# Optimization experiments

Measured on AMD Instinct MI355X. Metric: run time of the kernel, lower is better.

Reference implementation:

```python
import jax, jax.numpy as jnp
import numpy as np

N, E, H, NH, HD = 16384, 131072, 128, 8, 16
CUTOFF = 5.0
PATCH = H // 2  # 64, aggregation_custom effective patch dim


def setup_inputs() -> dict:
    key = jax.random.key(0)
    ks = jax.random.split(key, 24)
    w = lambda k, s: (jax.random.normal(k, s, dtype=jnp.float32) * 0.05)
    d = jax.random.normal(ks[5], (E, 3), dtype=jnp.float32)
    d = d / (jnp.linalg.norm(d, axis=-1, keepdims=True) + 1e-8)  # unit directions
    return {
        "x": jax.random.normal(ks[0], (N, H), dtype=jnp.float32),
        "vec": jax.random.normal(ks[1], (N, 3, H), dtype=jnp.float32),
        "edge_index": jax.random.randint(ks[2], (2, E), 0, N),
        "r_ij": jax.random.uniform(ks[3], (E,), dtype=jnp.float32) * CUTOFF,
        "f_ij": jax.random.normal(ks[4], (E, H), dtype=jnp.float32),
        "d_ij": d,
        "ln_g": jnp.ones((H,), jnp.float32), "ln_b": jnp.zeros((H,), jnp.float32),
        "Wq": w(ks[6], (H, H)), "bq": jnp.zeros((H,), jnp.float32),
        "Wk": w(ks[7], (H, H)), "bk": jnp.zeros((H,), jnp.float32),
        "Wv": w(ks[8], (H, H)), "bv": jnp.zeros((H,), jnp.float32),
        "Wdk": w(ks[9], (H, H)), "bdk": jnp.zeros((H,), jnp.float32),
        "Wdv": w(ks[10], (H, H)), "bdv": jnp.zeros((H,), jnp.float32),
        "Wvec": w(ks[11], (3 * H, H)),
        "Ws": w(ks[12], (2 * H, H)), "bs": jnp.zeros((2 * H,), jnp.float32),
        "Wo": w(ks[13], (3 * H, H)), "bo": jnp.zeros((3 * H,), jnp.float32),
        "Wf": w(ks[14], (H, H)), "bf": jnp.zeros((H,), jnp.float32),
        "Wwsrc": w(ks[15], (H, H)), "Wwtrg": w(ks[16], (H, H)),
        "Wagg": w(ks[17], (H, PATCH)),  # fc_all: Linear(64 -> 128, no bias)
        "agg_param": jnp.full((1,), 1e-5, dtype=jnp.float32),
    }


def _cutoff(r):
    return 0.5 * (jnp.cos(jnp.pi * r / CUTOFF) + 1.0) * (r < CUTOFF).astype(r.dtype)


def _vector_rejection(v, d):
    # v: [E,3,H], d: [E,3]
    proj = (v * d[:, :, None]).sum(axis=1, keepdims=True)  # [E,1,H]
    return v - proj * d[:, :, None]


def reference(x, vec, edge_index, r_ij, f_ij, d_ij, ln_g, ln_b,
              Wq, bq, Wk, bk, Wv, bv, Wdk, bdk, Wdv, bdv, Wvec,
              Ws, bs, Wo, bo, Wf, bf, Wwsrc, Wwtrg, Wagg, agg_param):
    silu = jax.nn.silu
    n = x.shape[0]
    # LayerNorm on x; VecLayerNorm with norm_type='none', trainable=False is identity
    mu = x.mean(-1, keepdims=True)
    var = ((x - mu) ** 2).mean(-1, keepdims=True)
    xn = (x - mu) / jnp.sqrt(var + 1e-5) * ln_g + ln_b

    q = (xn @ Wq.T + bq).reshape(n, NH, HD)
    k = (xn @ Wk.T + bk).reshape(n, NH, HD)
    v = (xn @ Wv.T + bv).reshape(n, NH, HD)
    dk = silu(f_ij @ Wdk.T + bdk).reshape(-1, NH, HD)
    dv = silu(f_ij @ Wdv.T + bdv).reshape(-1, NH, HD)

    vec1, vec2, vec3 = jnp.split(jnp.einsum('nch,oh->nco', vec, Wvec), 3, axis=-1)
    vec_dot = (vec1 * vec2).sum(axis=1)  # [N,H]

    src, dst = edge_index[0], edge_index[1]  # j, i
    # --- message ---
    attn = (q[dst] * k[src] * dk).sum(-1)                      # [E,NH]
    attn = silu(attn) * _cutoff(r_ij)[:, None]
    vmsg = (v[src] * dv * attn[:, :, None]).reshape(-1, H)     # [E,H]
    s1, s2 = jnp.split(silu(vmsg @ Ws.T + bs), 2, axis=1)
    vec_msg = vec[src] * s1[:, None, :] + s2[:, None, :] * d_ij[:, :, None]  # [E,3,H]

    # --- aggregation_custom on scalar messages ---
    e = vmsg.reshape(-1, 2, PATCH)                 # [E,2,64]
    ex = jnp.clip(jnp.einsum('epd,od->epo', e, Wagg), 0.0, 1.0)  # [E,2,128]
    gated = jnp.concatenate([(e * ex[:, :, :PATCH]).sum(1),
                             (e * ex[:, :, PATCH:]).sum(1)], axis=-1)  # [E,128]
    x_orig = jax.ops.segment_sum(vmsg, dst, num_segments=n)
    x_gate = jax.ops.segment_sum(gated, dst, num_segments=n)
    x_agg = jnp.abs(agg_param) * x_gate + x_orig
    vec_agg = jax.ops.segment_sum(vec_msg.reshape(-1, 3 * H), dst, num_segments=n).reshape(n, 3, H)

    # --- update ---
    o1, o2, o3 = jnp.split(x_agg @ Wo.T + bo, 3, axis=1)
    dx = vec_dot * o2 + o3
    dvec = vec3 * o1[:, None, :] + vec_agg

    # --- edge_update ---
    w1 = _vector_rejection(jnp.einsum('ech,oh->eco', vec[dst], Wwtrg), d_ij)
    w2 = _vector_rejection(jnp.einsum('ech,oh->eco', vec[src], Wwsrc), -d_ij)
    w_dot = (w1 * w2).sum(axis=1)  # [E,H]
    df_ij = silu(f_ij @ Wf.T + bf) * w_dot
    return dx, dvec, df_ij
```

## Files before the change

### kernel.cpp

```cpp
#include <hip/hip_runtime.h>

#define NN 16384
#define NE 131072
#define HH 128

typedef unsigned short u16;
typedef unsigned int u32;
typedef __attribute__((ext_vector_type(8))) short short8;
typedef __attribute__((ext_vector_type(4))) float f32x4;
typedef __attribute__((ext_vector_type(2))) float f32x2;
typedef __attribute__((ext_vector_type(2))) u32 u32x2;

__device__ __forceinline__ float b2f(u16 u){ u32 i=((u32)u)<<16; float f; __builtin_memcpy(&f,&i,4); return f; }
__device__ __forceinline__ u16 f2b(float f){ u32 i; __builtin_memcpy(&i,&f,4); u32 r=(i+0x7fffu+((i>>16)&1u))>>16; return (u16)r; }
__device__ __forceinline__ float blo(u32 v){ return b2f((u16)(v&0xffffu)); }
__device__ __forceinline__ float bhi(u32 v){ return b2f((u16)(v>>16)); }
__device__ __forceinline__ u32 pk(float a, float b){ return (u32)f2b(a) | ((u32)f2b(b)<<16); }
__device__ __forceinline__ float siluf(float x){ return x/(1.f+__expf(-x)); }

#define PBASE 58720256u
enum : unsigned {
  O_Wq=PBASE+0, O_Wk=PBASE+16384, O_Wv=PBASE+32768, O_Wdk=PBASE+49152,
  O_Wdv=PBASE+65536, O_Wf=PBASE+81920, O_Wwsrc=PBASE+98304, O_Wwtrg=PBASE+114688,
  O_Wvec=PBASE+131072, O_Ws=PBASE+180224, O_Wo=PBASE+212992, O_Wagg=PBASE+262144,
  O_bq=PBASE+270336, O_bk=PBASE+270464, O_bv=PBASE+270592, O_bdk=PBASE+270720,
  O_bdv=PBASE+270848, O_bs=PBASE+270976, O_bo=PBASE+271232, O_bf=PBASE+271616,
  O_lng=PBASE+271744, O_lnb=PBASE+271872, O_agg=PBASE+272000
};
#define CNT_OFF 117985280u
#define CUR_OFF 118050816u
#define SE_OFF  118116352u

struct Seg { const float* s; u32 off; u32 n; };
struct Pack { Seg d[25]; int cnt; };

__global__ __launch_bounds__(256) void k_cvt(Pack p, u16* __restrict__ base){
  int tid = blockIdx.x*blockDim.x + threadIdx.x;
  int stride = gridDim.x*blockDim.x;
  for (int s=0; s<p.cnt; ++s){
    const float* src = p.d[s].s;
    u16* dst = base + p.d[s].off;
    int n = (int)p.d[s].n, n4 = n>>2;
    const f32x4* s4 = (const f32x4*)src;
    for (int i=tid; i<n4; i+=stride){
      f32x4 v = s4[i];
      u32x2 o; o[0] = pk(v[0], v[1]); o[1] = pk(v[2], v[3]);
      *(u32x2*)(dst + 4*(size_t)i) = o;
    }
    for (int i = n4*4 + tid; i < n; i += stride) dst[i] = f2b(src[i]);
  }
}

__global__ __launch_bounds__(256) void k_hist(const int* __restrict__ ei, int* __restrict__ cnt){
  int e = blockIdx.x*256 + threadIdx.x;
  atomicAdd(&cnt[ei[NE + e]], 1);
}
__global__ __launch_bounds__(1024) void k_scan(const int* __restrict__ cnt, int* __restrict__ cur){
  __shared__ int part[1024];
  int t = threadIdx.x;
  int base = t*16;
  int local[16]; int s = 0;
#pragma unroll
  for (int k=0;k<16;++k){ local[k] = cnt[base+k]; s += local[k]; }
  part[t] = s;
  __syncthreads();
  for (int d=1; d<1024; d<<=1){
    int v = (t>=d) ? part[t-d] : 0;
    __syncthreads();
    part[t] += v;
    __syncthreads();
  }
  int run = (t>0) ? part[t-1] : 0;
#pragma unroll
  for (int k=0;k<16;++k){ cur[base+k] = run; run += local[k]; }
}
__global__ __launch_bounds__(256) void k_place(const int* __restrict__ ei, int* __restrict__ cur,
                                               int* __restrict__ se){
  int e = blockIdx.x*256 + threadIdx.x;
  int p = atomicAdd(&cur[ei[NE + e]], 1);
  se[p] = e;
}

template<int NK>
__device__ __forceinline__ f32x4 mm16(const u16* A, int lda, const u16* W, int ldw, f32x4 acc){
  int lane = threadIdx.x & 63;
  const u16* pa = A + (lane & 15)*lda + ((lane>>4)<<3);
  const u16* pw = W + (lane & 15)*ldw + ((lane>>4)<<3);
#pragma unroll
  for (int kc = 0; kc < NK; ++kc){
    short8 a = *(const short8*)(pa + kc*32);
    short8 b = *(const short8*)(pw + kc*32);
    acc = __builtin_amdgcn_mfma_f32_16x16x32_bf16(a, b, acc, 0, 0, 0);
  }
  return acc;
}

__global__ __launch_bounds__(256) void k_ln(const float* __restrict__ x, const u16* __restrict__ pb,
                                            u16* __restrict__ xn){
  int wid = threadIdx.x>>6, lane = threadIdx.x & 63;
  int n = blockIdx.x*4 + wid;
  f32x2 v = *(const f32x2*)(x + (size_t)n*HH + 2*lane);
  float a0 = v[0], a1 = v[1];
  float s = a0 + a1;
#pragma unroll
  for (int m=32; m; m>>=1) s += __shfl_xor(s, m);
  float mu = s*(1.f/128.f);
  float d0 = a0-mu, d1 = a1-mu;
  float vs = d0*d0 + d1*d1;
#pragma unroll
  for (int m=32; m; m>>=1) vs += __shfl_xor(vs, m);
  float rs = rsqrtf(vs*(1.f/128.f) + 1e-5f);
  u32 gg = *(const u32*)(pb + O_lng + 2*lane);
  u32 bb = *(const u32*)(pb + O_lnb + 2*lane);
  *(u32*)(xn + (size_t)n*HH + 2*lane) = pk(d0*rs*blo(gg)+blo(bb), d1*rs*bhi(gg)+bhi(bb));
}

__global__ __launch_bounds__(256) void k_gemm_qkv(const u16* __restrict__ xn,
    const u16* __restrict__ pb, u16* __restrict__ qkv){
  int wid = threadIdx.x>>6, lane = threadIdx.x & 63;
  int ct = blockIdx.y*4 + wid;
  int r0 = blockIdx.x*16;
  unsigned wo, bo_;
  if (ct < 8)      { wo = O_Wq; bo_ = O_bq; }
  else if (ct <16) { wo = O_Wk; bo_ = O_bk; }
  else             { wo = O_Wv; bo_ = O_bv; }
  int c0 = (ct & 7)*16;
  f32x4 acc = {0,0,0,0};
  acc = mm16<4>(xn + (size_t)r0*HH, HH, pb + wo + c0*HH, HH, acc);
  int col = ct*16 + (lane & 15);
  float bb = b2f(pb[bo_ + c0 + (lane&15)]);
#pragma unroll
  for (int j=0;j<4;++j){
    int r = r0 + ((lane>>4)<<2) + j;
    qkv[(size_t)r*384 + col] = f2b(acc[j] + bb);
  }
}

__global__ __launch_bounds__(256) void k_gemm_vec(const float* __restrict__ vecf,
    const u16* __restrict__ pb,
    u16* __restrict__ v12, u16* __restrict__ vec3, u16* __restrict__ Y){
  __shared__ u16 At[16*128];
  int tid = threadIdx.x, wid = tid>>6, lane = tid & 63;
  int r0 = blockIdx.x*16;
  {
    const float* src = vecf + (size_t)r0*HH;
    for (int i = tid*4; i < 2048; i += 1024){
      f32x4 v = *(const f32x4*)(src + i);
      u32x2 o; o[0] = pk(v[0], v[1]); o[1] = pk(v[2], v[3]);
      *(u32x2*)(At + i) = o;
    }
  }
  __syncthreads();
  for (int ct = wid; ct < 40; ct += 4){
    unsigned wo; int wc0;
    if (ct < 24)      { wo = O_Wvec;  wc0 = ct*16; }
    else if (ct < 32) { wo = O_Wwsrc; wc0 = (ct-24)*16; }
    else              { wo = O_Wwtrg; wc0 = (ct-32)*16; }
    f32x4 acc = {0,0,0,0};
    acc = mm16<4>(At, HH, pb + wo + wc0*HH, HH, acc);
    u16* dst; int ldc, dc0;
    if (ct < 16)      { dst = v12;  ldc = 256; dc0 = ct*16; }
    else if (ct < 24) { dst = vec3; ldc = 128; dc0 = (ct-16)*16; }
    else if (ct < 32) { dst = Y;    ldc = 256; dc0 = (ct-24)*16; }
    else              { dst = Y;    ldc = 256; dc0 = (ct-32)*16 + 128; }
    int col = dc0 + (lane & 15);
#pragma unroll
    for (int j=0;j<4;++j){
      int r = r0 + ((lane>>4)<<2) + j;
      dst[(size_t)r*ldc + col] = f2b(acc[j]);
    }
  }
}

__global__ __launch_bounds__(256) void k_edge(const float* __restrict__ f_ij,
    const u16* __restrict__ pb,
    const u16* __restrict__ qkv, const u16* __restrict__ Y,
    const int* __restrict__ ei, const int* __restrict__ se,
    const float* __restrict__ r_ij, const float* __restrict__ d_ij,
    const float* __restrict__ vecf, const float* __restrict__ aggf,
    float* __restrict__ df, float* __restrict__ xacc, float* __restrict__ vacc){
  __shared__ u16 fs[64*128];
  __shared__ u16 g2s[64*256];
  int tid = threadIdx.x, wid = tid>>6, lane = tid & 63;
  int t0 = blockIdx.x*64;
  int ereg=0, dreg=0, sreg=0;
  if (lane < 16){
    ereg = se[t0 + wid*16 + lane];
    dreg = ei[NE + ereg];
    sreg = ei[ereg];
  }
#pragma unroll
  for (int pass=0; pass<8; ++pass){
    int idx = pass*256 + lane*4;
    int rloc = idx >> 7, col = idx & 127;
    int er = __shfl(ereg, rloc);
    f32x4 v = *(const f32x4*)(f_ij + (size_t)er*HH + col);
    u32x2 o; o[0]=pk(v[0],v[1]); o[1]=pk(v[2],v[3]);
    *(u32x2*)(fs + (wid*16 + rloc)*HH + col) = o;
  }
  {
    const u16* pa = fs + (size_t)(wid*16 + (lane&15))*HH + ((lane>>4)<<3);
    short8 a0 = *(const short8*)(pa);
    short8 a1 = *(const short8*)(pa + 32);
    short8 a2 = *(const short8*)(pa + 64);
    short8 a3 = *(const short8*)(pa + 96);
    for (int ct=0; ct<16; ++ct){
      unsigned wo  = (ct<8) ? O_Wdk : O_Wdv;
      unsigned bo_ = (ct<8) ? O_bdk : O_bdv;
      int c0 = (ct&7)*16;
      const u16* pw = pb + wo + (size_t)(c0 + (lane&15))*HH + ((lane>>4)<<3);
      f32x4 acc = {0,0,0,0};
      acc = __builtin_amdgcn_mfma_f32_16x16x32_bf16(a0, *(const short8*)(pw),      acc, 0,0,0);
      acc = __builtin_amdgcn_mfma_f32_16x16x32_bf16(a1, *(const short8*)(pw + 32), acc, 0,0,0);
      acc = __builtin_amdgcn_mfma_f32_16x16x32_bf16(a2, *(const short8*)(pw + 64), acc, 0,0,0);
      acc = __builtin_amdgcn_mfma_f32_16x16x32_bf16(a3, *(const short8*)(pw + 96), acc, 0,0,0);
      float bb = b2f(pb[bo_ + c0 + (lane&15)]);
#pragma unroll
      for (int j=0;j<4;++j){
        int r = wid*16 + ((lane>>4)<<2) + j;
        g2s[r*256 + ct*16 + (lane&15)] = f2b(siluf(acc[j] + bb));
      }
    }
    f32x4 ffa[8];
#pragma unroll
    for (int cf=0; cf<8; ++cf){
      const u16* pw = pb + O_Wf + (size_t)(cf*16 + (lane&15))*HH + ((lane>>4)<<3);
      f32x4 acc = {0,0,0,0};
      acc = __builtin_amdgcn_mfma_f32_16x16x32_bf16(a0, *(const short8*)(pw),      acc, 0,0,0);
      acc = __builtin_amdgcn_mfma_f32_16x16x32_bf16(a1, *(const short8*)(pw + 32), acc, 0,0,0);
      acc = __builtin_amdgcn_mfma_f32_16x16x32_bf16(a2, *(const short8*)(pw + 64), acc, 0,0,0);
      acc = __builtin_amdgcn_mfma_f32_16x16x32_bf16(a3, *(const short8*)(pw + 96), acc, 0,0,0);
      ffa[cf] = acc;
    }
#pragma unroll
    for (int cf=0; cf<8; ++cf){
      float bb = b2f(pb[O_bf + cf*16 + (lane&15)]);
#pragma unroll
      for (int j=0;j<4;++j){
        int r = wid*16 + ((lane>>4)<<2) + j;
        fs[r*HH + cf*16 + (lane&15)] = f2b(siluf(ffa[cf][j] + bb));
      }
    }
  }
  int h0 = 2*lane;
  {
    int pdst = -1; u32 qq=0, ya0=0, ya1=0, ya2=0;
    for (int i=0;i<16;++i){
      int el = wid*16 + i;
      int e   = __shfl(ereg, i);
      int dst = __shfl(dreg, i);
      int src = __shfl(sreg, i);
      if (dst != pdst){
        qq  = *(const u32*)(qkv + (size_t)dst*384 + h0);
        ya0 = *(const u32*)(Y + ((size_t)dst*3+0)*256 + 128 + h0);
        ya1 = *(const u32*)(Y + ((size_t)dst*3+1)*256 + 128 + h0);
        ya2 = *(const u32*)(Y + ((size_t)dst*3+2)*256 + 128 + h0);
        pdst = dst;
      }
      u32 kk = *(const u32*)(qkv + (size_t)src*384 + 128 + h0);
      u32 vv = *(const u32*)(qkv + (size_t)src*384 + 256 + h0);
      u32 dk = *(const u32*)(g2s + el*256 + h0);
      u32 dv = *(const u32*)(g2s + el*256 + 128 + h0);
      u32 ff = *(const u32*)(fs  + el*HH + h0);
      float p = blo(qq)*blo(kk)*blo(dk) + bhi(qq)*bhi(kk)*bhi(dk);
      p += __shfl_xor(p,1); p += __shfl_xor(p,2); p += __shfl_xor(p,4);
      float r = r_ij[e];
      float cut = 0.5f*(__cosf(0.6283185307f*r)+1.f) * (r < 5.f ? 1.f : 0.f);
      float attn = siluf(p)*cut;
      float m0 = blo(vv)*blo(dv)*attn, m1 = bhi(vv)*bhi(dv)*attn;
      float ab0=0,ab1=0, ad0=0,ad1=0, bd0=0,bd1=0, ss=0;
      u32 ya[3] = {ya0, ya1, ya2};
#pragma unroll
      for (int c=0;c<3;++c){
        u32 bv2 = *(const u32*)(Y + ((size_t)src*3+c)*256 + h0);
        float dc = d_ij[(size_t)e*3+c];
        ab0 += blo(ya[c])*blo(bv2); ab1 += bhi(ya[c])*bhi(bv2);
        ad0 += blo(ya[c])*dc;       ad1 += bhi(ya[c])*dc;
        bd0 += blo(bv2)*dc;         bd1 += bhi(bv2)*dc;
        ss  += dc*dc;
      }
      float t = 2.f - ss;
      f32x2 dfo; dfo[0] = blo(ff)*(ab0 - ad0*bd0*t); dfo[1] = bhi(ff)*(ab1 - ad1*bd1*t);
      *(f32x2*)(df + (size_t)e*HH + h0) = dfo;
      *(u32*)(fs + el*HH + h0) = pk(m0, m1);
    }
  }
  float absA = fabsf(aggf[0]);
#pragma unroll
  for (int rr=0; rr<2; ++rr){
    int rt = wid*2 + rr;
    int el2 = wid*16 + 8*rr + ((lane&15)>>1);
    const u16* pa2 = fs + (size_t)el2*HH + ((lane&15)&1)*64 + ((lane>>4)<<3);
    short8 b0 = *(const short8*)(pa2);
    short8 b1 = *(const short8*)(pa2 + 32);
    for (int ct=0; ct<8; ++ct){
      const u16* pw = pb + O_Wagg + (size_t)(ct*16 + (lane&15))*64 + ((lane>>4)<<3);
      f32x4 acc = {0,0,0,0};
      acc = __builtin_amdgcn_mfma_f32_16x16x32_bf16(b0, *(const short8*)(pw),      acc, 0,0,0);
      acc = __builtin_amdgcn_mfma_f32_16x16x32_bf16(b1, *(const short8*)(pw + 32), acc, 0,0,0);
#pragma unroll
      for (int j=0;j<4;++j){
        int r = rt*16 + ((lane>>4)<<2) + j;
        g2s[r*128 + ct*16 + (lane&15)] = f2b(fminf(fmaxf(acc[j],0.f),1.f));
      }
    }
  }
  {
    int rdst = -1; float xc0=0.f, xc1=0.f;
    for (int i=0;i<16;++i){
      int el = wid*16 + i;
      int dst = __shfl(dreg, i);
      if (dst != rdst){
        if (rdst >= 0){
          atomicAdd(&xacc[(size_t)rdst*HH + h0],     xc0);
          atomicAdd(&xacc[(size_t)rdst*HH + h0 + 1], xc1);
        }
        rdst = dst; xc0 = xc1 = 0.f;
      }
      u32 mm = *(const u32*)(fs + el*HH + h0);
      u32 ml = *(const u32*)(fs + el*HH + (h0 & 63));
      u32 mh = *(const u32*)(fs + el*HH + 64 + (h0 & 63));
      u32 ex0 = *(const u32*)(g2s + (2*el)*128 + h0);
      u32 ex1 = *(const u32*)(g2s + (2*el+1)*128 + h0);
      xc0 += blo(mm) + absA*(blo(ml)*blo(ex0) + blo(mh)*blo(ex1));
      xc1 += bhi(mm) + absA*(bhi(ml)*bhi(ex0) + bhi(mh)*bhi(ex1));
    }
    if (rdst >= 0){
      atomicAdd(&xacc[(size_t)rdst*HH + h0],     xc0);
      atomicAdd(&xacc[(size_t)rdst*HH + h0 + 1], xc1);
    }
  }
  {
    const u16* ps = fs + (size_t)(wid*16 + (lane&15))*HH + ((lane>>4)<<3);
    short8 sa0 = *(const short8*)(ps);
    short8 sa1 = *(const short8*)(ps + 32);
    short8 sa2 = *(const short8*)(ps + 64);
    short8 sa3 = *(const short8*)(ps + 96);
    for (int ct=0; ct<16; ++ct){
      const u16* pw = pb + O_Ws + (size_t)(ct*16 + (lane&15))*HH + ((lane>>4)<<3);
      f32x4 acc = {0,0,0,0};
      acc = __builtin_amdgcn_mfma_f32_16x16x32_bf16(sa0, *(const short8*)(pw),      acc, 0,0,0);
      acc = __builtin_amdgcn_mfma_f32_16x16x32_bf16(sa1, *(const short8*)(pw + 32), acc, 0,0,0);
      acc = __builtin_amdgcn_mfma_f32_16x16x32_bf16(sa2, *(const short8*)(pw + 64), acc, 0,0,0);
      acc = __builtin_amdgcn_mfma_f32_16x16x32_bf16(sa3, *(const short8*)(pw + 96), acc, 0,0,0);
      float bb = b2f(pb[O_bs + ct*16 + (lane&15)]);
#pragma unroll
      for (int j=0;j<4;++j){
        int r = wid*16 + ((lane>>4)<<2) + j;
        g2s[r*256 + ct*16 + (lane&15)] = f2b(siluf(acc[j] + bb));
      }
    }
  }
  {
    int rdst = -1;
    float vc00=0.f,vc01=0.f, vc10=0.f,vc11=0.f, vc20=0.f,vc21=0.f;
    for (int i=0;i<16;++i){
      int el = wid*16 + i;
      int e   = __shfl(ereg, i);
      int dst = __shfl(dreg, i);
      int src = __shfl(sreg, i);
      if (dst != rdst){
        if (rdst >= 0){
          atomicAdd(&vacc[((size_t)rdst*3+0)*HH + h0],     vc00);
          atomicAdd(&vacc[((size_t)rdst*3+0)*HH + h0 + 1], vc01);
          atomicAdd(&vacc[((size_t)rdst*3+1)*HH + h0],     vc10);
          atomicAdd(&vacc[((size_t)rdst*3+1)*HH + h0 + 1], vc11);
          atomicAdd(&vacc[((size_t)rdst*3+2)*HH + h0],     vc20);
          atomicAdd(&vacc[((size_t)rdst*3+2)*HH + h0 + 1], vc21);
        }
        rdst = dst;
        vc00=vc01=vc10=vc11=vc20=vc21=0.f;
      }
      u32 s1 = *(const u32*)(g2s + el*256 + h0);
      u32 s2 = *(const u32*)(g2s + el*256 + 128 + h0);
      f32x2 vv0 = *(const f32x2*)(vecf + ((size_t)src*3+0)*HH + h0);
      f32x2 vv1 = *(const f32x2*)(vecf + ((size_t)src*3+1)*HH + h0);
      f32x2 vv2 = *(const f32x2*)(vecf + ((size_t)src*3+2)*HH + h0);
      float dc0 = d_ij[(size_t)e*3+0], dc1 = d_ij[(size_t)e*3+1], dc2 = d_ij[(size_t)e*3+2];
      vc00 += vv0[0]*blo(s1) + blo(s2)*dc0;  vc01 += vv0[1]*bhi(s1) + bhi(s2)*dc0;
      vc10 += vv1[0]*blo(s1) + blo(s2)*dc1;  vc11 += vv1[1]*bhi(s1) + bhi(s2)*dc1;
      vc20 += vv2[0]*blo(s1) + blo(s2)*dc2;  vc21 += vv2[1]*bhi(s1) + bhi(s2)*dc2;
    }
    if (rdst >= 0){
      atomicAdd(&vacc[((size_t)rdst*3+0)*HH + h0],     vc00);
      atomicAdd(&vacc[((size_t)rdst*3+0)*HH + h0 + 1], vc01);
      atomicAdd(&vacc[((size_t)rdst*3+1)*HH + h0],     vc10);
      atomicAdd(&vacc[((size_t)rdst*3+1)*HH + h0 + 1], vc11);
      atomicAdd(&vacc[((size_t)rdst*3+2)*HH + h0],     vc20);
      atomicAdd(&vacc[((size_t)rdst*3+2)*HH + h0 + 1], vc21);
    }
  }
}

__global__ __launch_bounds__(256) void k_update(const float* __restrict__ xacc,
    const u16* __restrict__ pb, const u16* __restrict__ v12, const u16* __restrict__ vec3,
    const float* __restrict__ vacc,
    float* __restrict__ dx, float* __restrict__ dvec){
  int wid = threadIdx.x>>6, lane = threadIdx.x & 63;
  int ct = blockIdx.y*4 + wid;
  int r0 = blockIdx.x*16;
  int c0 = ct*16;
  f32x4 a1 = {0,0,0,0}, a2 = {0,0,0,0}, a3 = {0,0,0,0};
  const float* pa = xacc + (size_t)(r0 + (lane&15))*HH + ((lane>>4)<<3);
#pragma unroll
  for (int kc=0; kc<4; ++kc){
    f32x4 f0 = *(const f32x4*)(pa + kc*32);
    f32x4 f1 = *(const f32x4*)(pa + kc*32 + 4);
    short8 av;
    av[0]=(short)f2b(f0[0]); av[1]=(short)f2b(f0[1]); av[2]=(short)f2b(f0[2]); av[3]=(short)f2b(f0[3]);
    av[4]=(short)f2b(f1[0]); av[5]=(short)f2b(f1[1]); av[6]=(short)f2b(f1[2]); av[7]=(short)f2b(f1[3]);
    const u16* pw = pb + O_Wo + (size_t)(c0 + (lane&15))*HH + ((lane>>4)<<3) + kc*32;
    short8 b1 = *(const short8*)(pw);
    short8 b2 = *(const short8*)(pw + 128*HH);
    short8 b3 = *(const short8*)(pw + 256*HH);
    a1 = __builtin_amdgcn_mfma_f32_16x16x32_bf16(av, b1, a1, 0,0,0);
    a2 = __builtin_amdgcn_mfma_f32_16x16x32_bf16(av, b2, a2, 0,0,0);
    a3 = __builtin_amdgcn_mfma_f32_16x16x32_bf16(av, b3, a3, 0,0,0);
  }
  int h = c0 + (lane & 15);
  float bo1 = b2f(pb[O_bo + h]), bo2 = b2f(pb[O_bo + 128 + h]), bo3 = b2f(pb[O_bo + 256 + h]);
#pragma unroll
  for (int j=0;j<4;++j){
    int r = r0 + ((lane>>4)<<2) + j;
    float o1 = a1[j]+bo1, o2 = a2[j]+bo2, o3 = a3[j]+bo3;
    float vdot = 0.f;
#pragma unroll
    for (int c=0;c<3;++c){
      const u16* row = v12 + ((size_t)r*3 + c)*256;
      vdot += b2f(row[h]) * b2f(row[128 + h]);
    }
    dx[(size_t)r*HH + h] = vdot*o2 + o3;
#pragma unroll
    for (int c=0;c<3;++c){
      size_t idx = ((size_t)r*3+c)*HH + h;
      dvec[idx] = b2f(vec3[idx])*o1 + vacc[idx];
    }
  }
}

extern "C" void kernel_launch(void* const* d_in, const int* in_sizes, int n_in,
                              void* d_out, int out_size, void* d_ws, size_t ws_size,
                              hipStream_t stream){
  (void)in_sizes; (void)n_in; (void)out_size; (void)ws_size;
  const float* x     = (const float*)d_in[0];
  const float* vecf  = (const float*)d_in[1];
  const int*   ei    = (const int*)d_in[2];
  const float* r_ij  = (const float*)d_in[3];
  const float* f_ij  = (const float*)d_in[4];
  const float* d_ij  = (const float*)d_in[5];
  const float* aggf  = (const float*)d_in[28];

  char* ws = (char*)d_ws;
  u16*   wsu   = (u16*)d_ws;
  float* xacc  = (float*)(ws + 0);
  float* vacc  = (float*)(ws + 8388608);
  u16*   Ybuf  = (u16*)(ws + 33554432);
  u16*   xn    = (u16*)(ws + 58720256);
  u16*   vec3  = (u16*)(ws + 67108864);
  u16*   qkv   = (u16*)(ws + 79691776);
  u16*   v12   = (u16*)(ws + 92274688);
  int*   cnt   = (int*)(ws + CNT_OFF);
  int*   cur   = (int*)(ws + CUR_OFF);
  int*   se    = (int*)(ws + SE_OFF);

  float* out  = (float*)d_out;
  float* dx   = out;
  float* dvec = out + (size_t)NN*128;
  float* df   = out + (size_t)NN*512;

  Pack p; int c = 0;
  auto add = [&](int idx, unsigned off, unsigned n){ p.d[c].s=(const float*)d_in[idx]; p.d[c].off=off; p.d[c].n=n; ++c; };
  add(8,  O_Wq,   16384); add(10, O_Wk,   16384); add(12, O_Wv,   16384);
  add(14, O_Wdk,  16384); add(16, O_Wdv,  16384); add(23, O_Wf,   16384);
  add(25, O_Wwsrc,16384); add(26, O_Wwtrg,16384);
  add(18, O_Wvec, 49152); add(19, O_Ws,   32768); add(21, O_Wo,   49152);
  add(27, O_Wagg,  8192);
  add(9,  O_bq, 128); add(11, O_bk, 128); add(13, O_bv, 128); add(15, O_bdk, 128);
  add(17, O_bdv, 128); add(20, O_bs, 256); add(22, O_bo, 384); add(24, O_bf, 128);
  add(6,  O_lng, 128); add(7,  O_lnb, 128); add(28, O_agg, 1);
  p.cnt = c;

  hipMemsetAsync(ws, 0, 33554432, stream);
  hipMemsetAsync(ws + CNT_OFF, 0, 65536, stream);
  k_hist<<<dim3(NE/256), 256, 0, stream>>>(ei, cnt);
  k_scan<<<dim3(1), 1024, 0, stream>>>(cnt, cur);
  k_place<<<dim3(NE/256), 256, 0, stream>>>(ei, cur, se);
  k_cvt<<<dim3(128), 256, 0, stream>>>(p, wsu);
  k_ln<<<dim3(NN/4), 256, 0, stream>>>(x, wsu, xn);
  k_gemm_qkv<<<dim3(NN/16, 6), 256, 0, stream>>>(xn, wsu, qkv);
  k_gemm_vec<<<dim3(3*NN/16), 256, 0, stream>>>(vecf, wsu, v12, vec3, Ybuf);
  k_edge<<<dim3(NE/64), 256, 0, stream>>>(f_ij, wsu, qkv, Ybuf, ei, se, r_ij, d_ij,
                                          vecf, aggf, df, xacc, vacc);
  k_update<<<dim3(NN/16, 2), 256, 0, stream>>>(xacc, wsu, v12, vec3, vacc, dx, dvec);
}
```

Baseline: 428.6 us.

## Swizzle LDS tiles and software-prefetch per-edge gathers in edge kernel

Applies an XOR swizzle to the byte addresses of the shared-memory tiles fs and g2s so that the MFMA fragment reads and the strided stores spread across LDS banks. It also prefetches the next edge's source-node gathers (k, v, Y, vec) and its r_ij and d_ij values one iteration ahead in the two per-edge loops, hiding global load latency. The prefetch adds register pressure, which could lower occupancy, and the swizzle adds a little address arithmetic.

```diff
diff --git a/kernel.cpp b/kernel.cpp
--- a/kernel.cpp
+++ b/kernel.cpp
@@ -17,6 +17,9 @@
 __device__ __forceinline__ float bhi(u32 v){ return b2f((u16)(v>>16)); }
 __device__ __forceinline__ u32 pk(float a, float b){ return (u32)f2b(a) | ((u32)f2b(b)<<16); }
 __device__ __forceinline__ float siluf(float x){ return x/(1.f+__expf(-x)); }
+
+#define SW8(b) ((b) ^ ((((b)>>8)&7)<<4))
+#define SW9(b) ((b) ^ ((((b)>>9)&7)<<4))
 
 #define PBASE 58720256u
 enum : unsigned {
@@ -181,6 +184,8 @@
     float* __restrict__ df, float* __restrict__ xacc, float* __restrict__ vacc){
   __shared__ u16 fs[64*128];
   __shared__ u16 g2s[64*256];
+  char* fsb  = (char*)fs;
+  char* g2b  = (char*)g2s;
   int tid = threadIdx.x, wid = tid>>6, lane = tid & 63;
   int t0 = blockIdx.x*64;
   int ereg=0, dreg=0, sreg=0;
@@ -196,14 +201,16 @@
     int er = __shfl(ereg, rloc);
     f32x4 v = *(const f32x4*)(f_ij + (size_t)er*HH + col);
     u32x2 o; o[0]=pk(v[0],v[1]); o[1]=pk(v[2],v[3]);
-    *(u32x2*)(fs + (wid*16 + rloc)*HH + col) = o;
+    int b = (wid*16 + rloc)*256 + col*2;
+    *(u32x2*)(fsb + SW8(b)) = o;
   }
   {
-    const u16* pa = fs + (size_t)(wid*16 + (lane&15))*HH + ((lane>>4)<<3);
-    short8 a0 = *(const short8*)(pa);
-    short8 a1 = *(const short8*)(pa + 32);
-    short8 a2 = *(const short8*)(pa + 64);
-    short8 a3 = *(const short8*)(pa + 96);
+    int arow = wid*16 + (lane&15);
+    int ab = arow*256 + ((lane>>4)<<4);
+    short8 a0 = *(const short8*)(fsb + SW8(ab));
+    short8 a1 = *(const short8*)(fsb + SW8(ab + 64));
+    short8 a2 = *(const short8*)(fsb + SW8(ab + 128));
+    short8 a3 = *(const short8*)(fsb + SW8(ab + 192));
     for (int ct=0; ct<16; ++ct){
       unsigned wo  = (ct<8) ? O_Wdk : O_Wdv;
       unsigned bo_ = (ct<8) ? O_bdk : O_bdv;
@@ -218,7 +225,8 @@
 #pragma unroll
       for (int j=0;j<4;++j){
         int r = wid*16 + ((lane>>4)<<2) + j;
-        g2s[r*256 + ct*16 + (lane&15)] = f2b(siluf(acc[j] + bb));
+        int b = r*512 + (ct*16 + (lane&15))*2;
+        *(u16*)(g2b + SW9(b)) = f2b(siluf(acc[j] + bb));
       }
     }
     f32x4 ffa[8];
@@ -238,18 +246,43 @@
 #pragma unroll
       for (int j=0;j<4;++j){
         int r = wid*16 + ((lane>>4)<<2) + j;
-        fs[r*HH + cf*16 + (lane&15)] = f2b(siluf(ffa[cf][j] + bb));
+        int b = r*256 + (cf*16 + (lane&15))*2;
+        *(u16*)(fsb + SW8(b)) = f2b(siluf(ffa[cf][j] + bb));
       }
     }
   }
   int h0 = 2*lane;
   {
     int pdst = -1; u32 qq=0, ya0=0, ya1=0, ya2=0;
+    int e_c = __shfl(ereg, 0), src_c = __shfl(sreg, 0);
+    u32 kk_c  = *(const u32*)(qkv + (size_t)src_c*384 + 128 + h0);
+    u32 vv_c  = *(const u32*)(qkv + (size_t)src_c*384 + 256 + h0);
+    u32 yb0_c = *(const u32*)(Y + ((size_t)src_c*3+0)*256 + h0);
+    u32 yb1_c = *(const u32*)(Y + ((size_t)src_c*3+1)*256 + h0);
+    u32 yb2_c = *(const u32*)(Y + ((size_t)src_c*3+2)*256 + h0);
+    float r_c   = r_ij[e_c];
+    float dc0_c = d_ij[(size_t)e_c*3+0];
+    float dc1_c = d_ij[(size_t)e_c*3+1];
+    float dc2_c = d_ij[(size_t)e_c*3+2];
     for (int i=0;i<16;++i){
+      int e = e_c;
+      u32 kk=kk_c, vv=vv_c, yb0=yb0_c, yb1=yb1_c, yb2=yb2_c;
+      float r=r_c, dc0=dc0_c, dc1=dc1_c, dc2=dc2_c;
+      if (i<15){
+        int e_n = __shfl(ereg, i+1), src_n = __shfl(sreg, i+1);
+        kk_c  = *(const u32*)(qkv + (size_t)src_n*384 + 128 + h0);
+        vv_c  = *(const u32*)(qkv + (size_t)src_n*384 + 256 + h0);
+        yb0_c = *(const u32*)(Y + ((size_t)src_n*3+0)*256 + h0);
+        yb1_c = *(const u32*)(Y + ((size_t)src_n*3+1)*256 + h0);
+        yb2_c = *(const u32*)(Y + ((size_t)src_n*3+2)*256 + h0);
+        r_c   = r_ij[e_n];
+        dc0_c = d_ij[(size_t)e_n*3+0];
+        dc1_c = d_ij[(size_t)e_n*3+1];
+        dc2_c = d_ij[(size_t)e_n*3+2];
+        e_c = e_n;
+      }
       int el = wid*16 + i;
-      int e   = __shfl(ereg, i);
       int dst = __shfl(dreg, i);
-      int src = __shfl(sreg, i);
       if (dst != pdst){
         qq  = *(const u32*)(qkv + (size_t)dst*384 + h0);
         ya0 = *(const u32*)(Y + ((size_t)dst*3+0)*256 + 128 + h0);
@@ -257,32 +290,33 @@
         ya2 = *(const u32*)(Y + ((size_t)dst*3+2)*256 + 128 + h0);
         pdst = dst;
       }
-      u32 kk = *(const u32*)(qkv + (size_t)src*384 + 128 + h0);
-      u32 vv = *(const u32*)(qkv + (size_t)src*384 + 256 + h0);
-      u32 dk = *(const u32*)(g2s + el*256 + h0);
-      u32 dv = *(const u32*)(g2s + el*256 + 128 + h0);
-      u32 ff = *(const u32*)(fs  + el*HH + h0);
+      int bdk = el*512 + h0*2;
+      u32 dk = *(const u32*)(g2b + SW9(bdk));
+      u32 dv = *(const u32*)(g2b + SW9(bdk + 256));
+      int bff = el*256 + h0*2;
+      u32 ff = *(const u32*)(fsb + SW8(bff));
       float p = blo(qq)*blo(kk)*blo(dk) + bhi(qq)*bhi(kk)*bhi(dk);
       p += __shfl_xor(p,1); p += __shfl_xor(p,2); p += __shfl_xor(p,4);
-      float r = r_ij[e];
       float cut = 0.5f*(__cosf(0.6283185307f*r)+1.f) * (r < 5.f ? 1.f : 0.f);
       float attn = siluf(p)*cut;
       float m0 = blo(vv)*blo(dv)*attn, m1 = bhi(vv)*bhi(dv)*attn;
-      float ab0=0,ab1=0, ad0=0,ad1=0, bd0=0,bd1=0, ss=0;
-      u32 ya[3] = {ya0, ya1, ya2};
-#pragma unroll
-      for (int c=0;c<3;++c){
-        u32 bv2 = *(const u32*)(Y + ((size_t)src*3+c)*256 + h0);
-        float dc = d_ij[(size_t)e*3+c];
-        ab0 += blo(ya[c])*blo(bv2); ab1 += bhi(ya[c])*bhi(bv2);
-        ad0 += blo(ya[c])*dc;       ad1 += bhi(ya[c])*dc;
-        bd0 += blo(bv2)*dc;         bd1 += bhi(bv2)*dc;
-        ss  += dc*dc;
-      }
+      float ab0,ab1, ad0,ad1, bd0,bd1, ss;
+      ab0 = blo(ya0)*blo(yb0); ab1 = bhi(ya0)*bhi(yb0);
+      ad0 = blo(ya0)*dc0;      ad1 = bhi(ya0)*dc0;
+      bd0 = blo(yb0)*dc0;      bd1 = bhi(yb0)*dc0;
+      ss  = dc0*dc0;
+      ab0 += blo(ya1)*blo(yb1); ab1 += bhi(ya1)*bhi(yb1);
+      ad0 += blo(ya1)*dc1;      ad1 += bhi(ya1)*dc1;
+      bd0 += blo(yb1)*dc1;      bd1 += bhi(yb1)*dc1;
+      ss  += dc1*dc1;
+      ab0 += blo(ya2)*blo(yb2); ab1 += bhi(ya2)*bhi(yb2);
+      ad0 += blo(ya2)*dc2;      ad1 += bhi(ya2)*dc2;
+      bd0 += blo(yb2)*dc2;      bd1 += bhi(yb2)*dc2;
+      ss  += dc2*dc2;
       float t = 2.f - ss;
       f32x2 dfo; dfo[0] = blo(ff)*(ab0 - ad0*bd0*t); dfo[1] = bhi(ff)*(ab1 - ad1*bd1*t);
       *(f32x2*)(df + (size_t)e*HH + h0) = dfo;
-      *(u32*)(fs + el*HH + h0) = pk(m0, m1);
+      *(u32*)(fsb + SW8(bff)) = pk(m0, m1);
     }
   }
   float absA = fabsf(aggf[0]);
@@ -290,9 +324,9 @@
   for (int rr=0; rr<2; ++rr){
     int rt = wid*2 + rr;
     int el2 = wid*16 + 8*rr + ((lane&15)>>1);
-    const u16* pa2 = fs + (size_t)el2*HH + ((lane&15)&1)*64 + ((lane>>4)<<3);
-    short8 b0 = *(const short8*)(pa2);
-    short8 b1 = *(const short8*)(pa2 + 32);
+    int pb2 = el2*256 + ((lane&15)&1)*128 + ((lane>>4)<<4);
+    short8 b0 = *(const short8*)(fsb + SW8(pb2));
+    short8 b1 = *(const short8*)(fsb + SW8(pb2 + 64));
     for (int ct=0; ct<8; ++ct){
       const u16* pw = pb + O_Wagg + (size_t)(ct*16 + (lane&15))*64 + ((lane>>4)<<3);
       f32x4 acc = {0,0,0,0};
@@ -301,7 +335,8 @@
 #pragma unroll
       for (int j=0;j<4;++j){
         int r = rt*16 + ((lane>>4)<<2) + j;
-        g2s[r*128 + ct*16 + (lane&15)] = f2b(fminf(fmaxf(acc[j],0.f),1.f));
+        int b = r*256 + (ct*16 + (lane&15))*2;
+        *(u16*)(g2b + SW8(b)) = f2b(fminf(fmaxf(acc[j],0.f),1.f));
       }
     }
   }
@@ -317,11 +352,12 @@
         }
         rdst = dst; xc0 = xc1 = 0.f;
       }
-      u32 mm = *(const u32*)(fs + el*HH + h0);
-      u32 ml = *(const u32*)(fs + el*HH + (h0 & 63));
-      u32 mh = *(const u32*)(fs + el*HH + 64 + (h0 & 63));
-      u32 ex0 = *(const u32*)(g2s + (2*el)*128 + h0);
-      u32 ex1 = *(const u32*)(g2s + (2*el+1)*128 + h0);
+      int bm = el*256;
+      u32 mm = *(const u32*)(fsb + SW8(bm + h0*2));
+      u32 ml = *(const u32*)(fsb + SW8(bm + (h0&63)*2));
+      u32 mh = *(const u32*)(fsb + SW8(bm + 128 + (h0&63)*2));
+      u32 ex0 = *(const u32*)(g2b + SW8((2*el)*256 + h0*2));
+      u32 ex1 = *(const u32*)(g2b + SW8((2*el+1)*256 + h0*2));
       xc0 += blo(mm) + absA*(blo(ml)*blo(ex0) + blo(mh)*blo(ex1));
       xc1 += bhi(mm) + absA*(bhi(ml)*bhi(ex0) + bhi(mh)*bhi(ex1));
     }
@@ -331,11 +367,12 @@
     }
   }
   {
-    const u16* ps = fs + (size_t)(wid*16 + (lane&15))*HH + ((lane>>4)<<3);
-    short8 sa0 = *(const short8*)(ps);
-    short8 sa1 = *(const short8*)(ps + 32);
-    short8 sa2 = *(const short8*)(ps + 64);
-    short8 sa3 = *(const short8*)(ps + 96);
+    int arow = wid*16 + (lane&15);
+    int ab = arow*256 + ((lane>>4)<<4);
+    short8 sa0 = *(const short8*)(fsb + SW8(ab));
+    short8 sa1 = *(const short8*)(fsb + SW8(ab + 64));
+    short8 sa2 = *(const short8*)(fsb + SW8(ab + 128));
+    short8 sa3 = *(const short8*)(fsb + SW8(ab + 192));
     for (int ct=0; ct<16; ++ct){
       const u16* pw = pb + O_Ws + (size_t)(ct*16 + (lane&15))*HH + ((lane>>4)<<3);
       f32x4 acc = {0,0,0,0};
@@ -347,18 +384,35 @@
 #pragma unroll
       for (int j=0;j<4;++j){
         int r = wid*16 + ((lane>>4)<<2) + j;
-        g2s[r*256 + ct*16 + (lane&15)] = f2b(siluf(acc[j] + bb));
+        int b = r*512 + (ct*16 + (lane&15))*2;
+        *(u16*)(g2b + SW9(b)) = f2b(siluf(acc[j] + bb));
       }
     }
   }
   {
     int rdst = -1;
     float vc00=0.f,vc01=0.f, vc10=0.f,vc11=0.f, vc20=0.f,vc21=0.f;
+    int e_c = __shfl(ereg, 0), src_c = __shfl(sreg, 0);
+    f32x2 v0_c = *(const f32x2*)(vecf + ((size_t)src_c*3+0)*HH + h0);
+    f32x2 v1_c = *(const f32x2*)(vecf + ((size_t)src_c*3+1)*HH + h0);
+    f32x2 v2_c = *(const f32x2*)(vecf + ((size_t)src_c*3+2)*HH + h0);
+    float dc0_c = d_ij[(size_t)e_c*3+0];
+    float dc1_c = d_ij[(size_t)e_c*3+1];
+    float dc2_c = d_ij[(size_t)e_c*3+2];
     for (int i=0;i<16;++i){
+      f32x2 vv0=v0_c, vv1=v1_c, vv2=v2_c;
+      float dc0=dc0_c, dc1=dc1_c, dc2=dc2_c;
+      if (i<15){
+        int e_n = __shfl(ereg, i+1), src_n = __shfl(sreg, i+1);
+        v0_c = *(const f32x2*)(vecf + ((size_t)src_n*3+0)*HH + h0);
+        v1_c = *(const f32x2*)(vecf + ((size_t)src_n*3+1)*HH + h0);
+        v2_c = *(const f32x2*)(vecf + ((size_t)src_n*3+2)*HH + h0);
+        dc0_c = d_ij[(size_t)e_n*3+0];
+        dc1_c = d_ij[(size_t)e_n*3+1];
+        dc2_c = d_ij[(size_t)e_n*3+2];
+      }
       int el = wid*16 + i;
-      int e   = __shfl(ereg, i);
       int dst = __shfl(dreg, i);
-      int src = __shfl(sreg, i);
       if (dst != rdst){
         if (rdst >= 0){
           atomicAdd(&vacc[((size_t)rdst*3+0)*HH + h0],     vc00);
@@ -371,12 +425,9 @@
         rdst = dst;
         vc00=vc01=vc10=vc11=vc20=vc21=0.f;
       }
-      u32 s1 = *(const u32*)(g2s + el*256 + h0);
-      u32 s2 = *(const u32*)(g2s + el*256 + 128 + h0);
-      f32x2 vv0 = *(const f32x2*)(vecf + ((size_t)src*3+0)*HH + h0);
-      f32x2 vv1 = *(const f32x2*)(vecf + ((size_t)src*3+1)*HH + h0);
-      f32x2 vv2 = *(const f32x2*)(vecf + ((size_t)src*3+2)*HH + h0);
-      float dc0 = d_ij[(size_t)e*3+0], dc1 = d_ij[(size_t)e*3+1], dc2 = d_ij[(size_t)e*3+2];
+      int bs1 = el*512 + h0*2;
+      u32 s1 = *(const u32*)(g2b + SW9(bs1));
+      u32 s2 = *(const u32*)(g2b + SW9(bs1 + 256));
       vc00 += vv0[0]*blo(s1) + blo(s2)*dc0;  vc01 += vv0[1]*bhi(s1) + bhi(s2)*dc0;
       vc10 += vv1[0]*blo(s1) + blo(s2)*dc1;  vc11 += vv1[1]*bhi(s1) + bhi(s2)*dc1;
       vc20 += vv2[0]*blo(s1) + blo(s2)*dc2;  vc21 += vv2[1]*bhi(s1) + bhi(s2)*dc2;
```

After: 421.2 us. Within noise of the previous version (-1.7%).
